# Kernel tuning notes

Measured on AMD Instinct MI355X. Metric: run time of the kernel, lower is better.

Reference implementation:

```python
import jax, jax.numpy as jnp
import numpy as np
from jax import lax

D_MODEL = 1024
D_STATE = 128
D_CONV = 4
EXPAND = 2
N_HEADS = 32
CHUNK = 64
D_INNER = EXPAND * D_MODEL                 # 2048
CONV_DIM = D_INNER + 2 * D_STATE           # 2304
D_IN_PROJ = 2 * D_INNER + 2 * D_STATE + N_HEADS  # 4384
HEAD_DIM = D_INNER // N_HEADS              # 64
EPS = 1e-5


def setup_inputs() -> dict:
    key = jax.random.key(0)
    ks = jax.random.split(key, 10)
    u = jax.random.normal(ks[0], (4, 4096, D_MODEL), dtype=jnp.float32)
    in_proj_w = jax.random.normal(ks[1], (D_IN_PROJ, D_MODEL), dtype=jnp.float32) * 0.02
    conv_w = jax.random.normal(ks[2], (CONV_DIM, 1, D_CONV), dtype=jnp.float32) * 0.3
    conv_b = jnp.zeros((CONV_DIM,), dtype=jnp.float32)
    dt_bias = jax.random.uniform(ks[3], (N_HEADS,), minval=-0.5, maxval=0.5, dtype=jnp.float32)
    A_log = jax.random.uniform(ks[4], (N_HEADS,), minval=-0.1, maxval=-0.01, dtype=jnp.float32)
    D = jax.random.uniform(ks[5], (N_HEADS,), minval=0.9, maxval=1.1, dtype=jnp.float32)
    norm_w = jnp.ones((D_INNER,), dtype=jnp.float32)
    out_proj_w = jax.random.normal(ks[6], (D_MODEL, D_INNER), dtype=jnp.float32) * 0.02
    return {"u": u, "in_proj_w": in_proj_w, "conv_w": conv_w, "conv_b": conv_b,
            "dt_bias": dt_bias, "A_log": A_log, "D": D, "norm_w": norm_w,
            "out_proj_w": out_proj_w}


def segsum(x):
    """Stable segment sum. x: (..., T) -> (..., T, T); exp of it is 1-semiseparable."""
    T = x.shape[-1]
    xe = jnp.broadcast_to(x[..., :, None], x.shape + (T,))  # '... d -> ... d e'
    mask_strict = jnp.tril(jnp.ones((T, T), dtype=bool), k=-1)
    xe = jnp.where(mask_strict, xe, 0.0)
    seg = jnp.cumsum(xe, axis=-2)
    mask_incl = jnp.tril(jnp.ones((T, T), dtype=bool), k=0)
    return jnp.where(mask_incl, seg, -jnp.inf)


def ssd(x, A, B, C):
    """x:(b,L,h,p)  A:(b,L,h)  B,C:(b,L,h,n). L multiple of CHUNK."""
    b, Lp, h, p = x.shape
    n = B.shape[-1]
    c = Lp // CHUNK
    x = x.reshape(b, c, CHUNK, h, p)
    A = A.reshape(b, c, CHUNK, h).transpose(0, 3, 1, 2)       # (b,h,c,l)
    B = B.reshape(b, c, CHUNK, h, n)
    C = C.reshape(b, c, CHUNK, h, n)
    A_cumsum = jnp.cumsum(A, axis=-1)                          # (b,h,c,l)
    L = jnp.exp(segsum(A))                                     # (b,h,c,l,l)
    # intra-chunk (diagonal blocks)
    Y_diag = jnp.einsum('bclhn,bcshn,bhcls,bcshp->bclhp', C, B, L, x)
    # chunk-final states
    decay_states = jnp.exp(A_cumsum[:, :, :, -1:] - A_cumsum)  # (b,h,c,l)
    states = jnp.einsum('bclhn,bhcl,bclhp->bchpn', B, decay_states, x)
    init = jnp.zeros_like(states[:, :1])
    states = jnp.concatenate([init, states], axis=1)           # (b,c+1,h,p,n)
    decay_chunk = jnp.exp(segsum(jnp.pad(A_cumsum[:, :, :, -1], ((0, 0), (0, 0), (1, 0)))))
    new_states = jnp.einsum('bhzc,bchpn->bzhpn', decay_chunk, states)
    states, final_state = new_states[:, :-1], new_states[:, -1]
    # inter-chunk (off-diagonal) contribution
    state_decay_out = jnp.exp(A_cumsum)
    Y_off = jnp.einsum('bclhn,bchpn,bhcl->bclhp', C, states, state_decay_out)
    Y = (Y_diag + Y_off).reshape(b, Lp, h, p)
    return Y, final_state


def _forward(u, in_proj_w, conv_w, conv_b, dt_bias, A_log, D, norm_w, out_proj_w):
    b, seq_len, _ = u.shape
    pad = CHUNK - seq_len % CHUNK  # note: full extra chunk when seq_len % CHUNK == 0 (faithful)
    u = jnp.pad(u, ((0, 0), (0, pad), (0, 0)))
    Lp = u.shape[1]
    A = -jnp.exp(A_log)                                        # (h,)
    zxbcdt = jnp.einsum('bld,ed->ble', u, in_proj_w)           # (b,Lp,D_IN_PROJ)
    z = zxbcdt[..., :D_INNER]
    xBC = zxbcdt[..., D_INNER:D_INNER + CONV_DIM]
    dt = zxbcdt[..., -N_HEADS:]
    # causal depthwise conv1d + silu
    xc = xBC.transpose(0, 2, 1)                                # (b,conv_dim,Lp)
    xc = lax.conv_general_dilated(xc, conv_w, window_strides=(1,),
                                  padding=[(D_CONV - 1, 0)],
                                  feature_group_count=CONV_DIM,
                                  dimension_numbers=('NCH', 'OIH', 'NCH'))
    xBC = jax.nn.silu((xc + conv_b[None, :, None]).transpose(0, 2, 1))
    x = xBC[..., :D_INNER].reshape(b, Lp, N_HEADS, HEAD_DIM)
    Bm = xBC[..., D_INNER:D_INNER + D_STATE]
    Cm = xBC[..., D_INNER + D_STATE:]
    Bm = jnp.broadcast_to(Bm[:, :, None, :], (b, Lp, N_HEADS, D_STATE))
    Cm = jnp.broadcast_to(Cm[:, :, None, :], (b, Lp, N_HEADS, D_STATE))
    dt = jax.nn.softplus(dt + dt_bias)                         # (b,Lp,h)
    y, _ = ssd(x * dt[..., None], A * dt, Bm, Cm)
    y = y + x * D[None, None, :, None]
    y = y.reshape(b, Lp, D_INNER)
    # gated RMSNorm
    t = y * jax.nn.silu(z)
    t = t * jax.lax.rsqrt(jnp.mean(t * t, axis=-1, keepdims=True) + EPS) * norm_w
    out = jnp.einsum('bld,ed->ble', t, out_proj_w)
    return out[:, :seq_len]


def reference(u, in_proj_w, conv_w, conv_b, dt_bias, A_log, D, norm_w, out_proj_w):
    return _forward(u, in_proj_w, conv_w, conv_b, dt_bias, A_log, D, norm_w, out_proj_w)
```

## Files before the change

kernel.cpp:

```cpp
#include <hip/hip_runtime.h>
#include <hip/hip_bf16.h>
#include <math.h>


#define BL    16384
#define NCONV 2304
#define LDXP  2336

typedef __hip_bfloat16 bf16;
typedef __attribute__((ext_vector_type(8))) short bf16x8_i;
typedef __attribute__((ext_vector_type(4))) float f32x4;

union BF8 { uint4 u; bf16 h[8]; };
union BF2 { uint u; bf16 h[2]; };

__device__ __forceinline__ void gload_lds16(const void* g, void* l) {
  __builtin_amdgcn_global_load_lds(
      (__attribute__((address_space(1))) void*)(uintptr_t)g,
      (__attribute__((address_space(3))) void*)(uint32_t)(uintptr_t)l,
      16, 0, 0);
}

template<typename TC, bool CLAMPB>
__global__ __launch_bounds__(256) void gemm_bt_mfma(
    const bf16* __restrict__ A, int lda,
    const bf16* __restrict__ B, int ldb,
    TC* __restrict__ C, int ldc, int N, int K)
{
  __shared__ __align__(16) bf16 As2[2][128 * 64];
  __shared__ __align__(16) bf16 Bs2[2][128 * 64];
  const int tid  = threadIdx.x;
  const int lane = tid & 63;
  const int wid  = tid >> 6;

  const int gx  = gridDim.x;
  const int nwg = gx * gridDim.y;
  const int q   = nwg >> 3;
  int id = blockIdx.y * gx + blockIdx.x;
  id = (id & 7) * q + (id >> 3);
  const int bm = (id / gx) * 128;
  const int bn = (id % gx) * 128;

  const int wr = (wid >> 1) * 64;
  const int wc = (wid & 1) * 64;

  f32x4 acc[4][4] = {};

  int aoff[4][2], boff[4][2];
  #pragma unroll
  for (int i = 0; i < 4; ++i) {
    const int ar = wr + i * 16 + (lane & 15);
    const int br = wc + i * 16 + (lane & 15);
    const int asw = ((ar >> 1) & 7) << 3;
    const int bsw = ((br >> 1) & 7) << 3;
    #pragma unroll
    for (int ks = 0; ks < 2; ++ks) {
      const int c0 = ks * 32 + (lane >> 4) * 8;
      aoff[i][ks] = ar * 64 + (c0 ^ asw);
      boff[i][ks] = br * 64 + (c0 ^ bsw);
    }
  }

  const int srow = tid >> 3;
  const int sj   = tid & 7;
  const bf16* pA[4];
  const bf16* pB[4];
  #pragma unroll
  for (int i = 0; i < 4; ++i) {
    const int r  = i * 32 + srow;
    const int js = sj ^ ((r >> 1) & 7);
    int brow = bn + r;
    if (CLAMPB) brow = min(brow, N - 1);
    pA[i] = A + (size_t)(bm + r) * lda + js * 8;
    pB[i] = B + (size_t)brow * ldb + js * 8;
  }

  const int NT = K >> 6;
  #pragma unroll
  for (int i = 0; i < 4; ++i) {
    gload_lds16(pA[i], &As2[0][0] + i * 2048 + wid * 512);
    gload_lds16(pB[i], &Bs2[0][0] + i * 2048 + wid * 512);
    pA[i] += 64; pB[i] += 64;
  }

  for (int t = 0; t < NT; ++t) {
    const int cur = t & 1;
    if (t + 1 < NT) {
      bf16* dA = &As2[cur ^ 1][0];
      bf16* dB = &Bs2[cur ^ 1][0];
      #pragma unroll
      for (int i = 0; i < 4; ++i) {
        gload_lds16(pA[i], dA + i * 2048 + wid * 512);
        gload_lds16(pB[i], dB + i * 2048 + wid * 512);
        pA[i] += 64; pB[i] += 64;
      }
      asm volatile("s_waitcnt vmcnt(8)" ::: "memory");
    } else {
      asm volatile("s_waitcnt vmcnt(0)" ::: "memory");
    }
    __builtin_amdgcn_sched_barrier(0);
    __builtin_amdgcn_s_barrier();
    const bf16* Ab = &As2[cur][0];
    const bf16* Bb = &Bs2[cur][0];
    __builtin_amdgcn_s_setprio(1);
    #pragma unroll
    for (int ks = 0; ks < 2; ++ks) {
      bf16x8_i af[4], bfr[4];
      #pragma unroll
      for (int i = 0; i < 4; ++i) {
        af[i]  = *(const bf16x8_i*)(Ab + aoff[i][ks]);
        bfr[i] = *(const bf16x8_i*)(Bb + boff[i][ks]);
      }
      #pragma unroll
      for (int i = 0; i < 4; ++i)
        #pragma unroll
        for (int j = 0; j < 4; ++j)
          acc[i][j] = __builtin_amdgcn_mfma_f32_16x16x32_bf16(
              af[i], bfr[j], acc[i][j], 0, 0, 0);
    }
    __builtin_amdgcn_s_setprio(0);
    __builtin_amdgcn_s_barrier();
  }

  const int cr = (lane >> 4) * 4;
  const int cc = lane & 15;
  #pragma unroll
  for (int i = 0; i < 4; ++i) {
    #pragma unroll
    for (int j = 0; j < 4; ++j) {
      const int n = bn + wc + j * 16 + cc;
      if (n < N) {
        #pragma unroll
        for (int r = 0; r < 4; ++r) {
          const int m = bm + wr + i * 16 + cr + r;
          if constexpr (sizeof(TC) == 2)
            ((bf16*)C)[(size_t)m * ldc + n] = __float2bfloat16(acc[i][j][r]);
          else
            ((float*)C)[(size_t)m * ldc + n] = acc[i][j][r];
        }
      }
    }
  }
}

__global__ __launch_bounds__(256) void cvt_f32_bf16(
    const float* __restrict__ in, bf16* __restrict__ out)
{
  const size_t i = (size_t)(blockIdx.x * 256 + threadIdx.x) * 8;
  float4 a = *(const float4*)(in + i);
  float4 b = *(const float4*)(in + i + 4);
  BF8 o;
  o.h[0] = __float2bfloat16(a.x); o.h[1] = __float2bfloat16(a.y);
  o.h[2] = __float2bfloat16(a.z); o.h[3] = __float2bfloat16(a.w);
  o.h[4] = __float2bfloat16(b.x); o.h[5] = __float2bfloat16(b.y);
  o.h[6] = __float2bfloat16(b.z); o.h[7] = __float2bfloat16(b.w);
  *(uint4*)(out + i) = o.u;
}

__global__ __launch_bounds__(256) void dtsp_atot_kernel(
    const bf16* __restrict__ xpre, const float* __restrict__ dt_bias,
    const float* __restrict__ A_log,
    float* __restrict__ dtT, float* __restrict__ Atot)
{
  const int c = blockIdx.x, b = blockIdx.y;
  const int tid = threadIdx.x;
  const int h = tid & 31, lg = tid >> 5;
  __shared__ float red[8][33];
  float s = 0.f, vals[8];
  const bf16* src = xpre + ((size_t)b * 4096 + c * 64 + lg * 8) * LDXP + 2304 + h;
  const float bias = dt_bias[h];
  #pragma unroll
  for (int k = 0; k < 8; ++k) {
    float v = __bfloat162float(src[(size_t)k * LDXP]) + bias;
    v = fmaxf(v, 0.f) + log1pf(expf(-fabsf(v)));
    vals[k] = v; s += v;
  }
  float* dp = dtT + ((size_t)(b * 32 + h)) * 4096 + c * 64 + lg * 8;
  #pragma unroll
  for (int k = 0; k < 8; ++k) dp[k] = vals[k];
  red[lg][h] = s;
  __syncthreads();
  if (tid < 32) {
    float t = 0.f;
    #pragma unroll
    for (int g = 0; g < 8; ++g) t += red[g][tid];
    Atot[((size_t)b * 64 + c) * 32 + tid] = -expf(A_log[tid]) * t;
  }
}

__global__ __launch_bounds__(256) void conv_silu_kernel(
    const bf16* __restrict__ xpre,
    const float* __restrict__ conv_w,
    const float* __restrict__ conv_b,
    bf16* __restrict__ xBC)
{
  const int ch = blockIdx.x * 256 + threadIdx.x;
  const int t0 = blockIdx.y * 8;
  const int bb = blockIdx.z;
  const float w0 = conv_w[ch*4+0], w1 = conv_w[ch*4+1];
  const float w2 = conv_w[ch*4+2], w3 = conv_w[ch*4+3];
  const float bias = conv_b[ch];
  const size_t rb = (size_t)bb * 4096;
  const bf16* src = xpre + ch;
  float v0 = (t0 >= 3) ? __bfloat162float(src[(rb + t0 - 3) * LDXP]) : 0.f;
  float v1 = (t0 >= 2) ? __bfloat162float(src[(rb + t0 - 2) * LDXP]) : 0.f;
  float v2 = (t0 >= 1) ? __bfloat162float(src[(rb + t0 - 1) * LDXP]) : 0.f;
  for (int t = t0; t < t0 + 8; ++t) {
    float v3 = __bfloat162float(src[(rb + t) * LDXP]);
    float o = bias + w0*v0 + w1*v1 + w2*v2 + w3*v3;
    o = o / (1.f + expf(-o));
    xBC[(rb + t) * NCONV + ch] = __float2bfloat16(o);
    v0 = v1; v1 = v2; v2 = v3;
  }
}

__device__ __forceinline__ int swz8(int row) { return ((row >> 3) & 7) << 3; }

__global__ __launch_bounds__(256) void s1_localstate(
    const bf16* __restrict__ xBC, const float* __restrict__ dtT,
    const float* __restrict__ A_log, bf16* __restrict__ states, int b)
{
  const int hh = blockIdx.x, c = blockIdx.y;
  const int tid = threadIdx.x, lane = tid & 63, wid = tid >> 6;
  __shared__ bf16 BT[128 * 72];
  __shared__ bf16 xwT[64 * 72];
  __shared__ bf16 Sout[64 * 136];
  const size_t r0 = (size_t)b * 4096 + (size_t)c * 64;

  BF8 regB[4], regx[2];
  #pragma unroll
  for (int k = 0; k < 4; ++k) {
    int id = tid + k * 256, l = id >> 4, n0 = (id & 15) * 8;
    regB[k].u = *(const uint4*)(xBC + (r0 + l) * NCONV + 2048 + n0);
  }
  #pragma unroll
  for (int k = 0; k < 2; ++k) {
    int id = tid + k * 256, l = id >> 3, p0 = (id & 7) * 8;
    regx[k].u = *(const uint4*)(xBC + (r0 + l) * NCONV + hh * 64 + p0);
  }

  float d = dtT[((size_t)(b * 32 + hh)) * 4096 + c * 64 + lane];
  float Ah = -expf(A_log[hh]);
  float v = Ah * d;
  #pragma unroll
  for (int off = 1; off < 64; off <<= 1) {
    float up = __shfl_up(v, off, 64);
    if (lane >= off) v += up;
  }
  const float At = __shfl(v, 63, 64);
  const float w = d * __expf(At - v);

  #pragma unroll
  for (int k = 0; k < 4; ++k) {
    int id = tid + k * 256, l = id >> 4, n0 = (id & 15) * 8;
    #pragma unroll
    for (int j = 0; j < 8; ++j) {
      int n = n0 + j;
      BT[n * 72 + (l ^ swz8(n))] = regB[k].h[j];
    }
  }
  #pragma unroll
  for (int k = 0; k < 2; ++k) {
    int id = tid + k * 256, l = id >> 3, p0 = (id & 7) * 8;
    float wv = __shfl(w, l, 64);
    #pragma unroll
    for (int j = 0; j < 8; ++j) {
      int p = p0 + j;
      xwT[p * 72 + (l ^ swz8(p))] =
          __float2bfloat16(__bfloat162float(regx[k].h[j]) * wv);
    }
  }
  __syncthreads();

  const int wr = (wid & 1) * 32;
  const int wc = (wid >> 1) * 64;
  f32x4 acc[2][4] = {};
  #pragma unroll
  for (int ks = 0; ks < 2; ++ks) {
    const int k0 = ks * 32 + (lane >> 4) * 8;
    bf16x8_i a[2], bb[4];
    #pragma unroll
    for (int i = 0; i < 2; ++i) {
      int p = wr + i * 16 + (lane & 15);
      a[i] = *(const bf16x8_i*)(xwT + p * 72 + (k0 ^ swz8(p)));
    }
    #pragma unroll
    for (int j = 0; j < 4; ++j) {
      int n = wc + j * 16 + (lane & 15);
      bb[j] = *(const bf16x8_i*)(BT + n * 72 + (k0 ^ swz8(n)));
    }
    #pragma unroll
    for (int i = 0; i < 2; ++i)
      #pragma unroll
      for (int j = 0; j < 4; ++j)
        acc[i][j] = __builtin_amdgcn_mfma_f32_16x16x32_bf16(
            a[i], bb[j], acc[i][j], 0, 0, 0);
  }

  const int cr = (lane >> 4) * 4, cn = lane & 15;
  #pragma unroll
  for (int i = 0; i < 2; ++i)
    #pragma unroll
    for (int j = 0; j < 4; ++j)
      #pragma unroll
      for (int r = 0; r < 4; ++r)
        Sout[(wr + i * 16 + cr + r) * 136 + (wc + j * 16 + cn)] =
            __float2bfloat16(acc[i][j][r]);
  __syncthreads();
  bf16* sb = states + ((size_t)c * 32 + hh) * 8192;
  #pragma unroll
  for (int k = 0; k < 4; ++k) {
    int id = tid + k * 256, p = id >> 4, n0 = (id & 15) * 8;
    *(uint4*)(sb + p * 128 + n0) = *(const uint4*)(Sout + p * 136 + n0);
  }
}

__global__ __launch_bounds__(256) void s2_scan(
    bf16* __restrict__ states, const float* __restrict__ Atot, int b)
{
  const int h  = blockIdx.x >> 4;
  const int p  = ((blockIdx.x & 15) << 2) | (threadIdx.x >> 6);
  const int n0 = (threadIdx.x & 63) * 2;
  __shared__ float ec[64];
  if (threadIdx.x < 64)
    ec[threadIdx.x] = expf(Atot[((size_t)b * 64 + threadIdx.x) * 32 + h]);
  __syncthreads();
  bf16* ptr = states + ((size_t)h * 64 + p) * 128 + n0;
  const size_t cs = (size_t)32 * 8192;
  float ca = 0.f, cb = 0.f;
  BF2 g0, g1, g2, g3, q0, q1, q2, q3;
  g0.u = *(const uint*)(ptr + 0 * cs);
  g1.u = *(const uint*)(ptr + 1 * cs);
  g2.u = *(const uint*)(ptr + 2 * cs);
  g3.u = *(const uint*)(ptr + 3 * cs);
  for (int g = 0; g < 16; ++g) {
    const int c0 = g * 4;
    if (g < 15) {
      q0.u = *(const uint*)(ptr + (c0 + 4) * cs);
      q1.u = *(const uint*)(ptr + (c0 + 5) * cs);
      q2.u = *(const uint*)(ptr + (c0 + 6) * cs);
      q3.u = *(const uint*)(ptr + (c0 + 7) * cs);
    }
    BF2 o0, o1, o2, o3;
    const float e0 = ec[c0], e1 = ec[c0+1], e2 = ec[c0+2], e3 = ec[c0+3];
    o0.h[0] = __float2bfloat16(ca); o0.h[1] = __float2bfloat16(cb);
    ca = fmaf(e0, ca, __bfloat162float(g0.h[0]));
    cb = fmaf(e0, cb, __bfloat162float(g0.h[1]));
    o1.h[0] = __float2bfloat16(ca); o1.h[1] = __float2bfloat16(cb);
    ca = fmaf(e1, ca, __bfloat162float(g1.h[0]));
    cb = fmaf(e1, cb, __bfloat162float(g1.h[1]));
    o2.h[0] = __float2bfloat16(ca); o2.h[1] = __float2bfloat16(cb);
    ca = fmaf(e2, ca, __bfloat162float(g2.h[0]));
    cb = fmaf(e2, cb, __bfloat162float(g2.h[1]));
    o3.h[0] = __float2bfloat16(ca); o3.h[1] = __float2bfloat16(cb);
    ca = fmaf(e3, ca, __bfloat162float(g3.h[0]));
    cb = fmaf(e3, cb, __bfloat162float(g3.h[1]));
    *(uint*)(ptr + (c0 + 0) * cs) = o0.u;
    *(uint*)(ptr + (c0 + 1) * cs) = o1.u;
    *(uint*)(ptr + (c0 + 2) * cs) = o2.u;
    *(uint*)(ptr + (c0 + 3) * cs) = o3.u;
    g0 = q0; g1 = q1; g2 = q2; g3 = q3;
  }
}

__global__ __launch_bounds__(256) void s3_output(
    const bf16* __restrict__ xBC, const float* __restrict__ dtT,
    const float* __restrict__ A_log, const float* __restrict__ Dp,
    const bf16* __restrict__ states, bf16* __restrict__ Y, int b)
{
  const int hh = blockIdx.x, c = blockIdx.y;
  const int tid = threadIdx.x, lane = tid & 63, wid = tid >> 6;
  __shared__ bf16 Cc[64 * 136];
  __shared__ bf16 Bc[64 * 136];
  __shared__ bf16 Sin[64 * 136];
  __shared__ bf16 xT[64 * 72];
  __shared__ bf16 scb[64 * 72];
  __shared__ float Ac[64], dts[64];
  const size_t r0 = (size_t)b * 4096 + (size_t)c * 64;

  if (tid < 64) {
    float d = dtT[((size_t)(b * 32 + hh)) * 4096 + c * 64 + tid];
    float Ah = -expf(A_log[hh]);
    float v = Ah * d;
    #pragma unroll
    for (int off = 1; off < 64; off <<= 1) {
      float up = __shfl_up(v, off, 64);
      if (tid >= off) v += up;
    }
    Ac[tid] = v; dts[tid] = d;
  }

  #pragma unroll
  for (int k = 0; k < 4; ++k) {
    int id = tid + k * 256, l = id >> 4, n0 = (id & 15) * 8;
    BF8 bv; bv.u = *(const uint4*)(xBC + (r0 + l) * NCONV + 2048 + n0);
    BF8 cv; cv.u = *(const uint4*)(xBC + (r0 + l) * NCONV + 2176 + n0);
    *(uint4*)(Bc + l * 136 + n0) = bv.u;
    *(uint4*)(Cc + l * 136 + n0) = cv.u;
  }
  const bf16* sb = states + ((size_t)c * 32 + hh) * 8192;
  #pragma unroll
  for (int k = 0; k < 4; ++k) {
    int id = tid + k * 256, p = id >> 4, n0 = (id & 15) * 8;
    *(uint4*)(Sin + p * 136 + n0) = *(const uint4*)(sb + p * 128 + n0);
  }
  #pragma unroll
  for (int k = 0; k < 2; ++k) {
    int id = tid + k * 256, l = id >> 3, p0 = (id & 7) * 8;
    BF8 v; v.u = *(const uint4*)(xBC + (r0 + l) * NCONV + hh * 64 + p0);
    #pragma unroll
    for (int j = 0; j < 8; ++j) {
      int p = p0 + j;
      xT[p * 72 + (l ^ swz8(p))] = v.h[j];
    }
  }
  __syncthreads();

  const int wr  = (wid & 1) * 32;
  const int wcs = (wid >> 1) * 32;
  f32x4 as[2][2] = {};
  bf16x8_i afrag[2][4];
  #pragma unroll
  for (int ks = 0; ks < 4; ++ks) {
    const int k0 = ks * 32 + (lane >> 4) * 8;
    #pragma unroll
    for (int i = 0; i < 2; ++i)
      afrag[i][ks] =
          *(const bf16x8_i*)(Cc + (wr + i * 16 + (lane & 15)) * 136 + k0);
    #pragma unroll
    for (int j = 0; j < 2; ++j) {
      bf16x8_i bfr =
          *(const bf16x8_i*)(Bc + (wcs + j * 16 + (lane & 15)) * 136 + k0);
      #pragma unroll
      for (int i = 0; i < 2; ++i)
        as[i][j] = __builtin_amdgcn_mfma_f32_16x16x32_bf16(
            afrag[i][ks], bfr, as[i][j], 0, 0, 0);
    }
  }
  const int cr = (lane >> 4) * 4, cc = lane & 15;
  #pragma unroll
  for (int i = 0; i < 2; ++i) {
    #pragma unroll
    for (int r = 0; r < 4; ++r) {
      const int l = wr + i * 16 + cr + r;
      const float acl = Ac[l];
      #pragma unroll
      for (int j = 0; j < 2; ++j) {
        const int s = wcs + j * 16 + cc;
        float val = (s <= l) ? as[i][j][r] * __expf(acl - Ac[s]) * dts[s] : 0.f;
        scb[l * 72 + s] = __float2bfloat16(val);
      }
    }
  }
  __syncthreads();

  f32x4 ay[2][2] = {};
  #pragma unroll
  for (int ks = 0; ks < 4; ++ks) {
    const int k0 = ks * 32 + (lane >> 4) * 8;
    #pragma unroll
    for (int j = 0; j < 2; ++j) {
      bf16x8_i bfr =
          *(const bf16x8_i*)(Sin + (wcs + j * 16 + (lane & 15)) * 136 + k0);
      #pragma unroll
      for (int i = 0; i < 2; ++i)
        ay[i][j] = __builtin_amdgcn_mfma_f32_16x16x32_bf16(
            afrag[i][ks], bfr, ay[i][j], 0, 0, 0);
    }
  }
  #pragma unroll
  for (int i = 0; i < 2; ++i)
    #pragma unroll
    for (int r = 0; r < 4; ++r) {
      const float dk = __expf(Ac[wr + i * 16 + cr + r]);
      #pragma unroll
      for (int j = 0; j < 2; ++j) ay[i][j][r] *= dk;
    }
  #pragma unroll
  for (int ks = 0; ks < 2; ++ks) {
    const int k0 = ks * 32 + (lane >> 4) * 8;
    bf16x8_i a2[2], b2[2];
    #pragma unroll
    for (int i = 0; i < 2; ++i)
      a2[i] = *(const bf16x8_i*)(scb + (wr + i * 16 + (lane & 15)) * 72 + k0);
    #pragma unroll
    for (int j = 0; j < 2; ++j) {
      int p = wcs + j * 16 + (lane & 15);
      b2[j] = *(const bf16x8_i*)(xT + p * 72 + (k0 ^ swz8(p)));
    }
    #pragma unroll
    for (int i = 0; i < 2; ++i)
      #pragma unroll
      for (int j = 0; j < 2; ++j)
        ay[i][j] = __builtin_amdgcn_mfma_f32_16x16x32_bf16(
            a2[i], b2[j], ay[i][j], 0, 0, 0);
  }
  const float Dh = Dp[hh];
  bf16* Yb = Bc;
  #pragma unroll
  for (int i = 0; i < 2; ++i)
    #pragma unroll
    for (int r = 0; r < 4; ++r) {
      const int l = wr + i * 16 + cr + r;
      #pragma unroll
      for (int j = 0; j < 2; ++j) {
        const int p = wcs + j * 16 + cc;
        float xv = __bfloat162float(xT[p * 72 + (l ^ swz8(p))]);
        Yb[l * 136 + p] = __float2bfloat16(ay[i][j][r] + Dh * xv);
      }
    }
  __syncthreads();
  #pragma unroll
  for (int k = 0; k < 2; ++k) {
    int id = tid + k * 256, l = id >> 3, p0 = (id & 7) * 8;
    *(uint4*)(Y + (r0 + l) * 2048 + hh * 64 + p0) =
        *(const uint4*)(Yb + l * 136 + p0);
  }
}

__global__ __launch_bounds__(256) void gate_rmsnorm_kernel(
    bf16* __restrict__ y, const bf16* __restrict__ z,
    const float* __restrict__ norm_w)
{
  const size_t row = blockIdx.x;
  const int tid = threadIdx.x;
  __shared__ float red[4];
  const bf16* zr = z + row * 2048;
  bf16* yr = y + row * 2048;
  BF8 zv, yv;
  zv.u = *(const uint4*)(zr + tid * 8);
  yv.u = *(const uint4*)(yr + tid * 8);
  float t[8];
  float local = 0.f;
  #pragma unroll
  for (int j = 0; j < 8; ++j) {
    float zz = __bfloat162float(zv.h[j]);
    float yy = __bfloat162float(yv.h[j]);
    float tv = yy * (zz / (1.f + expf(-zz)));
    t[j] = tv;
    local += tv * tv;
  }
  #pragma unroll
  for (int off = 32; off; off >>= 1) local += __shfl_down(local, off, 64);
  if ((tid & 63) == 0) red[tid >> 6] = local;
  __syncthreads();
  const float total = red[0] + red[1] + red[2] + red[3];
  const float scale = rsqrtf(total * (1.f / 2048.f) + 1e-5f);
  BF8 o;
  #pragma unroll
  for (int j = 0; j < 8; ++j)
    o.h[j] = __float2bfloat16(t[j] * scale * norm_w[tid * 8 + j]);
  *(uint4*)(yr + tid * 8) = o.u;
}

extern "C" void kernel_launch(void* const* d_in, const int* in_sizes, int n_in,
                              void* d_out, int out_size, void* d_ws, size_t ws_size,
                              hipStream_t stream) {
  (void)in_sizes; (void)n_in; (void)out_size; (void)ws_size;
  const float* u          = (const float*)d_in[0];
  const float* in_proj_w  = (const float*)d_in[1];
  const float* conv_w     = (const float*)d_in[2];
  const float* conv_b     = (const float*)d_in[3];
  const float* dt_bias    = (const float*)d_in[4];
  const float* A_log      = (const float*)d_in[5];
  const float* Dp         = (const float*)d_in[6];
  const float* norm_w     = (const float*)d_in[7];
  const float* out_proj_w = (const float*)d_in[8];
  float* out = (float*)d_out;

  char* ws = (char*)d_ws;
  bf16*  u_bf   = (bf16*)ws;
  bf16*  xpre   = (bf16*)(ws + 33554432);
  bf16*  xBCc   = (bf16*)(ws + 110100480);
  float* dtT    = (float*)(ws + 185597952);
  bf16*  W_xpre = (bf16*)(ws + 187695104);
  bf16*  W_z    = (bf16*)(ws + 192479232);
  bf16*  w_out  = (bf16*)(ws + 196673536);
  float* Atot   = (float*)(ws + 200867840);
  bf16*  states = (bf16*)(ws + 200900608);
  bf16*  ybuf   = xpre;
  bf16*  zbuf   = xBCc;

  cvt_f32_bf16<<<dim3(8192), 256, 0, stream>>>(u, u_bf);
  cvt_f32_bf16<<<dim3(1168), 256, 0, stream>>>(in_proj_w + (size_t)2048*1024,
                                               W_xpre);
  cvt_f32_bf16<<<dim3(1024), 256, 0, stream>>>(in_proj_w, W_z);
  cvt_f32_bf16<<<dim3(1024), 256, 0, stream>>>(out_proj_w, w_out);
  gemm_bt_mfma<bf16, true><<<dim3(19, 128), 256, 0, stream>>>(
      u_bf, 1024, W_xpre, 1024, xpre, LDXP, 2336, 1024);
  dtsp_atot_kernel<<<dim3(64, 4), 256, 0, stream>>>(xpre, dt_bias, A_log,
                                                    dtT, Atot);
  conv_silu_kernel<<<dim3(9, 512, 4), 256, 0, stream>>>(xpre, conv_w, conv_b,
                                                        xBCc);
  for (int b = 0; b < 4; ++b) {
    s1_localstate<<<dim3(32, 64), 256, 0, stream>>>(xBCc, dtT, A_log,
                                                    states, b);
    s2_scan<<<dim3(512), 256, 0, stream>>>(states, Atot, b);
    s3_output<<<dim3(32, 64), 256, 0, stream>>>(xBCc, dtT, A_log, Dp,
                                                states, ybuf, b);
  }
  gemm_bt_mfma<bf16, false><<<dim3(16, 128), 256, 0, stream>>>(
      u_bf, 1024, W_z, 1024, zbuf, 2048, 2048, 1024);
  gate_rmsnorm_kernel<<<dim3(BL), 256, 0, stream>>>(ybuf, zbuf, norm_w);
  gemm_bt_mfma<float, false><<<dim3(8, 128), 256, 0, stream>>>(
      ybuf, 2048, w_out, 2048, out, 1024, 1024, 2048);
}
```

Baseline: 529.7 us.

## Replace 128x128 GEMM with 256x256 tile, 8-wave kernel and staged half-tile prefetch

The bf16 MFMA GEMM goes from 128x128 tiles with 4 waves to 256x256 tiles with 8 waves (512 threads). Each wave computes 128x64, and the next K-tile's A and B halves are loaded in four staggered pieces between the four MFMA sub-phases. The aim is more operand reuse per LDS byte and less global traffic, with loads overlapped against compute. In exchange there are more barriers per K-step, higher register use for 32 accumulators, and far fewer workgroups (e.g. 256 for the out-projection), which may underfill the CUs.

```diff
diff --git a/kernel.cpp b/kernel.cpp
--- a/kernel.cpp
+++ b/kernel.cpp
@@ -22,125 +22,212 @@
 }
 
 template<typename TC, bool CLAMPB>
-__global__ __launch_bounds__(256) void gemm_bt_mfma(
+__global__ __launch_bounds__(512) void gemm_bt_256(
     const bf16* __restrict__ A, int lda,
     const bf16* __restrict__ B, int ldb,
     TC* __restrict__ C, int ldc, int N, int K)
 {
-  __shared__ __align__(16) bf16 As2[2][128 * 64];
-  __shared__ __align__(16) bf16 Bs2[2][128 * 64];
+  __shared__ __align__(16) bf16 As[2][2][8192];
+  __shared__ __align__(16) bf16 Bs[2][2][8192];
   const int tid  = threadIdx.x;
   const int lane = tid & 63;
   const int wid  = tid >> 6;
+  const int wm   = wid >> 2;
+  const int wn   = wid & 3;
 
   const int gx  = gridDim.x;
   const int nwg = gx * gridDim.y;
   const int q   = nwg >> 3;
   int id = blockIdx.y * gx + blockIdx.x;
   id = (id & 7) * q + (id >> 3);
-  const int bm = (id / gx) * 128;
-  const int bn = (id % gx) * 128;
-
-  const int wr = (wid >> 1) * 64;
-  const int wc = (wid & 1) * 64;
-
-  f32x4 acc[4][4] = {};
-
-  int aoff[4][2], boff[4][2];
-  #pragma unroll
-  for (int i = 0; i < 4; ++i) {
-    const int ar = wr + i * 16 + (lane & 15);
-    const int br = wc + i * 16 + (lane & 15);
-    const int asw = ((ar >> 1) & 7) << 3;
-    const int bsw = ((br >> 1) & 7) << 3;
-    #pragma unroll
-    for (int ks = 0; ks < 2; ++ks) {
-      const int c0 = ks * 32 + (lane >> 4) * 8;
-      aoff[i][ks] = ar * 64 + (c0 ^ asw);
-      boff[i][ks] = br * 64 + (c0 ^ bsw);
-    }
+  const int bm = (id / gx) * 256;
+  const int bn = (id % gx) * 256;
+
+  f32x4 acc[8][4] = {};
+
+  int aoff[2][4][2], boff[4][2];
+  #pragma unroll
+  for (int fh = 0; fh < 2; ++fh)
+    #pragma unroll
+    for (int mf = 0; mf < 4; ++mf) {
+      const int row = fh * 64 + mf * 16 + (lane & 15);
+      const int sw  = ((row >> 1) & 7) << 3;
+      #pragma unroll
+      for (int kh = 0; kh < 2; ++kh)
+        aoff[fh][mf][kh] = row * 64 + ((kh * 32 + (lane >> 4) * 8) ^ sw);
+    }
+  #pragma unroll
+  for (int nf = 0; nf < 4; ++nf) {
+    const int row = (wn & 1) * 64 + nf * 16 + (lane & 15);
+    const int sw  = ((row >> 1) & 7) << 3;
+    #pragma unroll
+    for (int kh = 0; kh < 2; ++kh)
+      boff[nf][kh] = row * 64 + ((kh * 32 + (lane >> 4) * 8) ^ sw);
   }
 
   const int srow = tid >> 3;
-  const int sj   = tid & 7;
-  const bf16* pA[4];
-  const bf16* pB[4];
-  #pragma unroll
-  for (int i = 0; i < 4; ++i) {
-    const int r  = i * 32 + srow;
-    const int js = sj ^ ((r >> 1) & 7);
-    int brow = bn + r;
-    if (CLAMPB) brow = min(brow, N - 1);
-    pA[i] = A + (size_t)(bm + r) * lda + js * 8;
-    pB[i] = B + (size_t)brow * ldb + js * 8;
-  }
+  const int js   = (tid & 7) ^ ((srow >> 1) & 7);
+  const int jcol = js * 8;
 
   const int NT = K >> 6;
   #pragma unroll
-  for (int i = 0; i < 4; ++i) {
-    gload_lds16(pA[i], &As2[0][0] + i * 2048 + wid * 512);
-    gload_lds16(pB[i], &Bs2[0][0] + i * 2048 + wid * 512);
-    pA[i] += 64; pB[i] += 64;
-  }
-
-  for (int t = 0; t < NT; ++t) {
-    const int cur = t & 1;
-    if (t + 1 < NT) {
-      bf16* dA = &As2[cur ^ 1][0];
-      bf16* dB = &Bs2[cur ^ 1][0];
-      #pragma unroll
-      for (int i = 0; i < 4; ++i) {
-        gload_lds16(pA[i], dA + i * 2048 + wid * 512);
-        gload_lds16(pB[i], dB + i * 2048 + wid * 512);
-        pA[i] += 64; pB[i] += 64;
+  for (int h = 0; h < 2; ++h)
+    #pragma unroll
+    for (int i = 0; i < 2; ++i) {
+      const int ra = bm + h * 128 + i * 64 + srow;
+      gload_lds16(A + (size_t)ra * lda + jcol,
+                  &As[0][h][0] + i * 4096 + wid * 512);
+      int rb = bn + h * 128 + i * 64 + srow;
+      if (CLAMPB) rb = min(rb, N - 1);
+      gload_lds16(B + (size_t)rb * ldb + jcol,
+                  &Bs[0][h][0] + i * 4096 + wid * 512);
+    }
+
+  for (int T = 0; T < NT; ++T) {
+    const int cur = T & 1;
+    const int k1  = (T + 1) << 6;
+    const bool st = (T + 1 < NT);
+    const bf16* Ah = &As[cur][wm][0];
+    const bf16* Bh = &Bs[cur][wn >> 1][0];
+    bf16x8_i bfr[4];
+
+    if (st) {
+      #pragma unroll
+      for (int i = 0; i < 2; ++i) {
+        const int ra = bm + i * 64 + srow;
+        gload_lds16(A + (size_t)ra * lda + k1 + jcol,
+                    &As[cur ^ 1][0][0] + i * 4096 + wid * 512);
       }
-      asm volatile("s_waitcnt vmcnt(8)" ::: "memory");
+      asm volatile("s_waitcnt vmcnt(2)" ::: "memory");
     } else {
       asm volatile("s_waitcnt vmcnt(0)" ::: "memory");
     }
     __builtin_amdgcn_sched_barrier(0);
     __builtin_amdgcn_s_barrier();
-    const bf16* Ab = &As2[cur][0];
-    const bf16* Bb = &Bs2[cur][0];
-    __builtin_amdgcn_s_setprio(1);
-    #pragma unroll
-    for (int ks = 0; ks < 2; ++ks) {
-      bf16x8_i af[4], bfr[4];
-      #pragma unroll
-      for (int i = 0; i < 4; ++i) {
-        af[i]  = *(const bf16x8_i*)(Ab + aoff[i][ks]);
-        bfr[i] = *(const bf16x8_i*)(Bb + boff[i][ks]);
+    {
+      bf16x8_i af[4];
+      #pragma unroll
+      for (int mf = 0; mf < 4; ++mf)
+        af[mf] = *(const bf16x8_i*)(Ah + aoff[0][mf][0]);
+      #pragma unroll
+      for (int nf = 0; nf < 4; ++nf)
+        bfr[nf] = *(const bf16x8_i*)(Bh + boff[nf][0]);
+      asm volatile("s_waitcnt lgkmcnt(0)" ::: "memory");
+      __builtin_amdgcn_sched_barrier(0);
+      __builtin_amdgcn_s_setprio(1);
+      #pragma unroll
+      for (int mf = 0; mf < 4; ++mf)
+        #pragma unroll
+        for (int nf = 0; nf < 4; ++nf)
+          acc[mf][nf] = __builtin_amdgcn_mfma_f32_16x16x32_bf16(
+              af[mf], bfr[nf], acc[mf][nf], 0, 0, 0);
+      __builtin_amdgcn_s_setprio(0);
+    }
+    __builtin_amdgcn_s_barrier();
+    if (st) {
+      #pragma unroll
+      for (int i = 0; i < 2; ++i) {
+        const int ra = bm + 128 + i * 64 + srow;
+        gload_lds16(A + (size_t)ra * lda + k1 + jcol,
+                    &As[cur ^ 1][1][0] + i * 4096 + wid * 512);
       }
-      #pragma unroll
-      for (int i = 0; i < 4; ++i)
+    }
+    {
+      bf16x8_i af[4];
+      #pragma unroll
+      for (int mf = 0; mf < 4; ++mf)
+        af[mf] = *(const bf16x8_i*)(Ah + aoff[1][mf][0]);
+      asm volatile("s_waitcnt lgkmcnt(0)" ::: "memory");
+      __builtin_amdgcn_sched_barrier(0);
+      __builtin_amdgcn_s_setprio(1);
+      #pragma unroll
+      for (int mf = 0; mf < 4; ++mf)
         #pragma unroll
-        for (int j = 0; j < 4; ++j)
-          acc[i][j] = __builtin_amdgcn_mfma_f32_16x16x32_bf16(
-              af[i], bfr[j], acc[i][j], 0, 0, 0);
-    }
-    __builtin_amdgcn_s_setprio(0);
+        for (int nf = 0; nf < 4; ++nf)
+          acc[4 + mf][nf] = __builtin_amdgcn_mfma_f32_16x16x32_bf16(
+              af[mf], bfr[nf], acc[4 + mf][nf], 0, 0, 0);
+      __builtin_amdgcn_s_setprio(0);
+    }
+    __builtin_amdgcn_s_barrier();
+    if (st) {
+      #pragma unroll
+      for (int i = 0; i < 2; ++i) {
+        int rb = bn + i * 64 + srow;
+        if (CLAMPB) rb = min(rb, N - 1);
+        gload_lds16(B + (size_t)rb * ldb + k1 + jcol,
+                    &Bs[cur ^ 1][0][0] + i * 4096 + wid * 512);
+      }
+    }
+    {
+      bf16x8_i af[4];
+      #pragma unroll
+      for (int mf = 0; mf < 4; ++mf)
+        af[mf] = *(const bf16x8_i*)(Ah + aoff[0][mf][1]);
+      #pragma unroll
+      for (int nf = 0; nf < 4; ++nf)
+        bfr[nf] = *(const bf16x8_i*)(Bh + boff[nf][1]);
+      asm volatile("s_waitcnt lgkmcnt(0)" ::: "memory");
+      __builtin_amdgcn_sched_barrier(0);
+      __builtin_amdgcn_s_setprio(1);
+      #pragma unroll
+      for (int mf = 0; mf < 4; ++mf)
+        #pragma unroll
+        for (int nf = 0; nf < 4; ++nf)
+          acc[mf][nf] = __builtin_amdgcn_mfma_f32_16x16x32_bf16(
+              af[mf], bfr[nf], acc[mf][nf], 0, 0, 0);
+      __builtin_amdgcn_s_setprio(0);
+    }
+    __builtin_amdgcn_s_barrier();
+    if (st) {
+      #pragma unroll
+      for (int i = 0; i < 2; ++i) {
+        int rb = bn + 128 + i * 64 + srow;
+        if (CLAMPB) rb = min(rb, N - 1);
+        gload_lds16(B + (size_t)rb * ldb + k1 + jcol,
+                    &Bs[cur ^ 1][1][0] + i * 4096 + wid * 512);
+      }
+    }
+    {
+      bf16x8_i af[4];
+      #pragma unroll
+      for (int mf = 0; mf < 4; ++mf)
+        af[mf] = *(const bf16x8_i*)(Ah + aoff[1][mf][1]);
+      asm volatile("s_waitcnt lgkmcnt(0)" ::: "memory");
+      __builtin_amdgcn_sched_barrier(0);
+      __builtin_amdgcn_s_setprio(1);
+      #pragma unroll
+      for (int mf = 0; mf < 4; ++mf)
+        #pragma unroll
+        for (int nf = 0; nf < 4; ++nf)
+          acc[4 + mf][nf] = __builtin_amdgcn_mfma_f32_16x16x32_bf16(
+              af[mf], bfr[nf], acc[4 + mf][nf], 0, 0, 0);
+      __builtin_amdgcn_s_setprio(0);
+    }
     __builtin_amdgcn_s_barrier();
   }
 
   const int cr = (lane >> 4) * 4;
   const int cc = lane & 15;
   #pragma unroll
-  for (int i = 0; i < 4; ++i) {
-    #pragma unroll
-    for (int j = 0; j < 4; ++j) {
-      const int n = bn + wc + j * 16 + cc;
-      if (n < N) {
-        #pragma unroll
-        for (int r = 0; r < 4; ++r) {
-          const int m = bm + wr + i * 16 + cr + r;
-          if constexpr (sizeof(TC) == 2)
-            ((bf16*)C)[(size_t)m * ldc + n] = __float2bfloat16(acc[i][j][r]);
-          else
-            ((float*)C)[(size_t)m * ldc + n] = acc[i][j][r];
+  for (int fh = 0; fh < 2; ++fh)
+    #pragma unroll
+    for (int mf = 0; mf < 4; ++mf) {
+      #pragma unroll
+      for (int nf = 0; nf < 4; ++nf) {
+        const int n = bn + wn * 64 + nf * 16 + cc;
+        if (n < N) {
+          #pragma unroll
+          for (int r = 0; r < 4; ++r) {
+            const int m = bm + wm * 128 + fh * 64 + mf * 16 + cr + r;
+            if constexpr (sizeof(TC) == 2)
+              ((bf16*)C)[(size_t)m * ldc + n] =
+                  __float2bfloat16(acc[fh * 4 + mf][nf][r]);
+            else
+              ((float*)C)[(size_t)m * ldc + n] = acc[fh * 4 + mf][nf][r];
+          }
         }
       }
     }
-  }
 }
 
 __global__ __launch_bounds__(256) void cvt_f32_bf16(
@@ -586,7 +673,7 @@
                                                W_xpre);
   cvt_f32_bf16<<<dim3(1024), 256, 0, stream>>>(in_proj_w, W_z);
   cvt_f32_bf16<<<dim3(1024), 256, 0, stream>>>(out_proj_w, w_out);
-  gemm_bt_mfma<bf16, true><<<dim3(19, 128), 256, 0, stream>>>(
+  gemm_bt_256<bf16, true><<<dim3(10, 64), 512, 0, stream>>>(
       u_bf, 1024, W_xpre, 1024, xpre, LDXP, 2336, 1024);
   dtsp_atot_kernel<<<dim3(64, 4), 256, 0, stream>>>(xpre, dt_bias, A_log,
                                                     dtT, Atot);
@@ -599,9 +686,9 @@
     s3_output<<<dim3(32, 64), 256, 0, stream>>>(xBCc, dtT, A_log, Dp,
                                                 states, ybuf, b);
   }
-  gemm_bt_mfma<bf16, false><<<dim3(16, 128), 256, 0, stream>>>(
+  gemm_bt_256<bf16, false><<<dim3(8, 64), 512, 0, stream>>>(
       u_bf, 1024, W_z, 1024, zbuf, 2048, 2048, 1024);
   gate_rmsnorm_kernel<<<dim3(BL), 256, 0, stream>>>(ybuf, zbuf, norm_w);
-  gemm_bt_mfma<float, false><<<dim3(8, 128), 256, 0, stream>>>(
+  gemm_bt_256<float, false><<<dim3(4, 64), 512, 0, stream>>>(
       ybuf, 2048, w_out, 2048, out, 1024, 1024, 2048);
 }
```

Measured after the change: 540.7 us. +2.1%, slower.

## Precompute head-shared C·Bᵀ chunk scores once instead of per head

Applied to the files above, without the earlier changes.

Since B and C are shared across all 32 heads, the intra-chunk C·Bᵀ score matrix is identical for every head. A new s0_scores kernel computes it once per (batch, chunk) into an fp32 workspace buffer, and s3_output reads it back instead of loading B and recomputing the MFMA per head. This removes 32x redundant matmul work and the B tile load per block. In exchange it adds an extra kernel launch plus fp32 global traffic of 16 KB per chunk read by every head block. It also reuses workspace memory at an offset that must not overlap live buffers.

```diff
diff --git a/kernel.cpp b/kernel.cpp
--- a/kernel.cpp
+++ b/kernel.cpp
@@ -215,6 +215,56 @@
 }
 
 __device__ __forceinline__ int swz8(int row) { return ((row >> 3) & 7) << 3; }
+
+__global__ __launch_bounds__(256) void s0_scores(
+    const bf16* __restrict__ xBC, float* __restrict__ sc_raw)
+{
+  const int c = blockIdx.x, b = blockIdx.y;
+  const int tid = threadIdx.x, lane = tid & 63, wid = tid >> 6;
+  __shared__ bf16 Bc[64 * 136];
+  __shared__ bf16 Cc[64 * 136];
+  const size_t r0 = (size_t)b * 4096 + (size_t)c * 64;
+  #pragma unroll
+  for (int k = 0; k < 4; ++k) {
+    int id = tid + k * 256, l = id >> 4, n0 = (id & 15) * 8;
+    *(uint4*)(Bc + l * 136 + n0) =
+        *(const uint4*)(xBC + (r0 + l) * NCONV + 2048 + n0);
+    *(uint4*)(Cc + l * 136 + n0) =
+        *(const uint4*)(xBC + (r0 + l) * NCONV + 2176 + n0);
+  }
+  __syncthreads();
+  const int wr  = (wid & 1) * 32;
+  const int wcs = (wid >> 1) * 32;
+  f32x4 as[2][2] = {};
+  #pragma unroll
+  for (int ks = 0; ks < 4; ++ks) {
+    const int k0 = ks * 32 + (lane >> 4) * 8;
+    bf16x8_i af[2], bfr[2];
+    #pragma unroll
+    for (int i = 0; i < 2; ++i)
+      af[i] = *(const bf16x8_i*)(Cc + (wr + i * 16 + (lane & 15)) * 136 + k0);
+    #pragma unroll
+    for (int j = 0; j < 2; ++j)
+      bfr[j] = *(const bf16x8_i*)(Bc + (wcs + j * 16 + (lane & 15)) * 136 + k0);
+    #pragma unroll
+    for (int i = 0; i < 2; ++i)
+      #pragma unroll
+      for (int j = 0; j < 2; ++j)
+        as[i][j] = __builtin_amdgcn_mfma_f32_16x16x32_bf16(
+            af[i], bfr[j], as[i][j], 0, 0, 0);
+  }
+  float* dst = sc_raw + ((size_t)(b * 64 + c)) * 4096;
+  const int cr = (lane >> 4) * 4, cc = lane & 15;
+  #pragma unroll
+  for (int i = 0; i < 2; ++i)
+    #pragma unroll
+    for (int r = 0; r < 4; ++r) {
+      const int l = wr + i * 16 + cr + r;
+      #pragma unroll
+      for (int j = 0; j < 2; ++j)
+        dst[l * 64 + wcs + j * 16 + cc] = as[i][j][r];
+    }
+}
 
 __global__ __launch_bounds__(256) void s1_localstate(
     const bf16* __restrict__ xBC, const float* __restrict__ dtT,
@@ -366,12 +416,13 @@
 __global__ __launch_bounds__(256) void s3_output(
     const bf16* __restrict__ xBC, const float* __restrict__ dtT,
     const float* __restrict__ A_log, const float* __restrict__ Dp,
-    const bf16* __restrict__ states, bf16* __restrict__ Y, int b)
+    const bf16* __restrict__ states, const float* __restrict__ sc_raw,
+    bf16* __restrict__ Y, int b)
 {
   const int hh = blockIdx.x, c = blockIdx.y;
   const int tid = threadIdx.x, lane = tid & 63, wid = tid >> 6;
   __shared__ bf16 Cc[64 * 136];
-  __shared__ bf16 Bc[64 * 136];
+  __shared__ bf16 Yb[64 * 136];
   __shared__ bf16 Sin[64 * 136];
   __shared__ bf16 xT[64 * 72];
   __shared__ bf16 scb[64 * 72];
@@ -393,10 +444,8 @@
   #pragma unroll
   for (int k = 0; k < 4; ++k) {
     int id = tid + k * 256, l = id >> 4, n0 = (id & 15) * 8;
-    BF8 bv; bv.u = *(const uint4*)(xBC + (r0 + l) * NCONV + 2048 + n0);
-    BF8 cv; cv.u = *(const uint4*)(xBC + (r0 + l) * NCONV + 2176 + n0);
-    *(uint4*)(Bc + l * 136 + n0) = bv.u;
-    *(uint4*)(Cc + l * 136 + n0) = cv.u;
+    *(uint4*)(Cc + l * 136 + n0) =
+        *(const uint4*)(xBC + (r0 + l) * NCONV + 2176 + n0);
   }
   const bf16* sb = states + ((size_t)c * 32 + hh) * 8192;
   #pragma unroll
@@ -418,7 +467,6 @@
 
   const int wr  = (wid & 1) * 32;
   const int wcs = (wid >> 1) * 32;
-  f32x4 as[2][2] = {};
   bf16x8_i afrag[2][4];
   #pragma unroll
   for (int ks = 0; ks < 4; ++ks) {
@@ -427,27 +475,20 @@
     for (int i = 0; i < 2; ++i)
       afrag[i][ks] =
           *(const bf16x8_i*)(Cc + (wr + i * 16 + (lane & 15)) * 136 + k0);
-    #pragma unroll
-    for (int j = 0; j < 2; ++j) {
-      bf16x8_i bfr =
-          *(const bf16x8_i*)(Bc + (wcs + j * 16 + (lane & 15)) * 136 + k0);
-      #pragma unroll
-      for (int i = 0; i < 2; ++i)
-        as[i][j] = __builtin_amdgcn_mfma_f32_16x16x32_bf16(
-            afrag[i][ks], bfr, as[i][j], 0, 0, 0);
-    }
-  }
-  const int cr = (lane >> 4) * 4, cc = lane & 15;
-  #pragma unroll
-  for (int i = 0; i < 2; ++i) {
-    #pragma unroll
-    for (int r = 0; r < 4; ++r) {
-      const int l = wr + i * 16 + cr + r;
+  }
+  {
+    const float* scr = sc_raw + ((size_t)(b * 64 + c)) * 4096;
+    #pragma unroll
+    for (int k = 0; k < 4; ++k) {
+      int idx = tid + k * 256;
+      int l = idx >> 4, s0 = (idx & 15) * 4;
+      float4 v = *(const float4*)(scr + l * 64 + s0);
       const float acl = Ac[l];
-      #pragma unroll
-      for (int j = 0; j < 2; ++j) {
-        const int s = wcs + j * 16 + cc;
-        float val = (s <= l) ? as[i][j][r] * __expf(acl - Ac[s]) * dts[s] : 0.f;
+      float vv[4] = {v.x, v.y, v.z, v.w};
+      #pragma unroll
+      for (int j = 0; j < 4; ++j) {
+        int s = s0 + j;
+        float val = (s <= l) ? vv[j] * __expf(acl - Ac[s]) * dts[s] : 0.f;
         scb[l * 72 + s] = __float2bfloat16(val);
       }
     }
@@ -468,6 +509,7 @@
             afrag[i][ks], bfr, ay[i][j], 0, 0, 0);
     }
   }
+  const int cr = (lane >> 4) * 4, cc = lane & 15;
   #pragma unroll
   for (int i = 0; i < 2; ++i)
     #pragma unroll
@@ -496,7 +538,6 @@
             a2[i], b2[j], ay[i][j], 0, 0, 0);
   }
   const float Dh = Dp[hh];
-  bf16* Yb = Bc;
   #pragma unroll
   for (int i = 0; i < 2; ++i)
     #pragma unroll
@@ -580,6 +621,7 @@
   bf16*  states = (bf16*)(ws + 200900608);
   bf16*  ybuf   = xpre;
   bf16*  zbuf   = xBCc;
+  float* sc_raw = (float*)(ws + 100663296);
 
   cvt_f32_bf16<<<dim3(8192), 256, 0, stream>>>(u, u_bf);
   cvt_f32_bf16<<<dim3(1168), 256, 0, stream>>>(in_proj_w + (size_t)2048*1024,
@@ -592,12 +634,13 @@
                                                     dtT, Atot);
   conv_silu_kernel<<<dim3(9, 512, 4), 256, 0, stream>>>(xpre, conv_w, conv_b,
                                                         xBCc);
+  s0_scores<<<dim3(64, 4), 256, 0, stream>>>(xBCc, sc_raw);
   for (int b = 0; b < 4; ++b) {
     s1_localstate<<<dim3(32, 64), 256, 0, stream>>>(xBCc, dtT, A_log,
                                                     states, b);
     s2_scan<<<dim3(512), 256, 0, stream>>>(states, Atot, b);
     s3_output<<<dim3(32, 64), 256, 0, stream>>>(xBCc, dtT, A_log, Dp,
-                                                states, ybuf, b);
+                                                states, sc_raw, ybuf, b);
   }
   gemm_bt_mfma<bf16, false><<<dim3(16, 128), 256, 0, stream>>>(
       u_bf, 1024, W_z, 1024, zbuf, 2048, 2048, 1024);
```

Measured after the change: 521.7 us. No clear change (-1.5%).
